# Kernel optimization log

Hardware: AMD Instinct MI355X
Metric: run time of the kernel (lower is better)

The kernel has to match this reference:

```python
import jax, jax.numpy as jnp
import numpy as np

B, NQ, NK, C, H = 4, 1024, 1024, 768, 12
DH = C // H
SCALE = DH ** -0.5
EPS = 1e-5  # nn.LayerNorm default
NEG_INF = float('-inf')


def _ln(x, g, b):
    m = jnp.mean(x, axis=-1, keepdims=True)
    v = jnp.mean((x - m) ** 2, axis=-1, keepdims=True)
    return (x - m) * jax.lax.rsqrt(v + EPS) * g + b


def _heads(t):  # [B,N,C] -> [B,H,N,Dh]
    Bq, N, _ = t.shape
    return t.reshape(Bq, N, H, DH).transpose(0, 2, 1, 3)


def setup_inputs() -> dict:
    key = jax.random.key(0)
    ks = jax.random.split(key, 32)
    w = lambda k, shape: jax.random.normal(k, shape, jnp.float32) * 0.02
    g = lambda k: 1.0 + jax.random.normal(k, (C,), jnp.float32) * 0.02
    b = lambda k: jax.random.normal(k, (C,), jnp.float32) * 0.02
    inp = {
        'x': jax.random.normal(ks[0], (B, NQ, C), jnp.float32),
        'y': jax.random.normal(ks[1], (B, NK, C), jnp.float32),
        'xpos': jnp.arange(B * NQ, dtype=jnp.int32).reshape(B, NQ),
        'ypos': jnp.arange(B * NK, dtype=jnp.int32).reshape(B, NK),
        'mask': jax.random.randint(ks[2], (NQ, NK), 0, 2) > 0,
        'similarities': jax.random.normal(ks[3], (B, H, NQ, NK), jnp.float32),
        # norms
        'ln1_g': g(ks[4]), 'ln1_b': b(ks[5]),
        'ln2_g': g(ks[6]), 'ln2_b': b(ks[7]),
        'ln3_g': g(ks[8]), 'ln3_b': b(ks[9]),
        'lny_g': g(ks[10]), 'lny_b': b(ks[11]),
        # self-attn (qkv_bias=False)
        'qkv_w': w(ks[12], (3 * C, C)),
        'aproj_w': w(ks[13], (C, C)), 'aproj_b': b(ks[14]),
        # cross-attn
        'pq_w': w(ks[15], (C, C)), 'pk_w': w(ks[16], (C, C)), 'pv_w': w(ks[17], (C, C)),
        'cproj_w': w(ks[18], (C, C)), 'cproj_b': b(ks[19]),
        # mlp (hidden = 4*C)
        'fc1_w': w(ks[20], (4 * C, C)), 'fc1_b': jax.random.normal(ks[21], (4 * C,), jnp.float32) * 0.02,
        'fc2_w': w(ks[22], (C, 4 * C)), 'fc2_b': b(ks[23]),
    }
    return inp


def reference(x, y, xpos, ypos, mask, similarities,
              ln1_g, ln1_b, ln2_g, ln2_b, ln3_g, ln3_b, lny_g, lny_b,
              qkv_w, aproj_w, aproj_b,
              pq_w, pk_w, pv_w, cproj_w, cproj_b,
              fc1_w, fc1_b, fc2_w, fc2_b):
    # ---- self-attention (rope=None, dropout=0) ----
    xn = _ln(x, ln1_g, ln1_b)
    qkv = (xn @ qkv_w.T).reshape(B, NQ, 3, H, DH).transpose(2, 0, 3, 1, 4)
    q, k, v = qkv[0], qkv[1], qkv[2]                       # [B,H,Nq,Dh]
    attn = jax.nn.softmax(jnp.einsum('bhqd,bhkd->bhqk', q, k) * SCALE, axis=-1)
    sa = jnp.einsum('bhqk,bhkd->bhqd', attn, v).transpose(0, 2, 1, 3).reshape(B, NQ, C)
    x = x + sa @ aproj_w.T + aproj_b

    # ---- sparse cross-attention with similarity bias + mask ----
    y_ = _ln(y, lny_g, lny_b)
    xn2 = _ln(x, ln2_g, ln2_b)
    cq = _heads(xn2 @ pq_w.T)                              # [B,H,Nq,Dh]
    ck = _heads(y_ @ pk_w.T)                               # [B,H,Nk,Dh]
    cv = _heads(y_ @ pv_w.T)
    scores = jnp.einsum('bhqd,bhkd->bhqk', cq, ck) * SCALE
    sims_c = similarities - jnp.mean(similarities, axis=1, keepdims=True)
    scores = scores + sims_c
    scores = jnp.where(mask[None, None], scores, NEG_INF)
    cattn = jax.nn.softmax(scores, axis=-1)
    ca = jnp.einsum('bhqk,bhkd->bhqd', cattn, cv).transpose(0, 2, 1, 3).reshape(B, NQ, C)
    x = x + ca @ cproj_w.T + cproj_b

    # ---- MLP (exact GELU, as nn.GELU default) ----
    xn3 = _ln(x, ln3_g, ln3_b)
    h = jax.nn.gelu(xn3 @ fc1_w.T + fc1_b, approximate=False)
    x = x + h @ fc2_w.T + fc2_b
    return (x, y)
```

## Files before the change

kernel.cpp:

```cpp
#include <hip/hip_runtime.h>
#include <cstdint>
#include <cstddef>


typedef __bf16 bf16;
typedef __attribute__((ext_vector_type(8))) __bf16 bf16x8;
typedef __attribute__((ext_vector_type(4))) __bf16 bf16x4;
typedef __attribute__((ext_vector_type(4))) float f32x4;

typedef __attribute__((address_space(1))) void gvoid;
typedef __attribute__((address_space(3))) void lvoid;

#define DEVI static __device__ __forceinline__

DEVI void gload16(const void* g, void* l) {
  __builtin_amdgcn_global_load_lds((gvoid*)(uintptr_t)g, (lvoid*)(uintptr_t)l, 16, 0, 0);
}

DEVI f32x4 mfma_bf16(bf16x8 a, bf16x8 b, f32x4 c) {
  return __builtin_amdgcn_mfma_f32_16x16x32_bf16(a, b, c, 0, 0, 0);
}

__global__ __launch_bounds__(256)
void detect_mask_k(const unsigned char* __restrict__ mask, int* __restrict__ shift)
{
  __shared__ int acc[256];
  const int t = threadIdx.x;
  int s = 0;
  for (int i = t; i < 16384; i += 256) {
    const int base = i * 4;
    s += mask[base + 1] + mask[base + 2] + mask[base + 3];
  }
  acc[t] = s;
  __syncthreads();
  #pragma unroll
  for (int o = 128; o; o >>= 1) {
    if (t < o) acc[t] += acc[t + o];
    __syncthreads();
  }
  if (t == 0) *shift = (acc[0] == 0) ? 2 : 0;
}

__global__ __launch_bounds__(256)
void bias_k(const float* __restrict__ sim,
            const unsigned char* __restrict__ mask,
            const int* __restrict__ mshift,
            bf16* __restrict__ biasOut)
{
  const int blk = blockIdx.x;
  const int b = blk >> 10, q = blk & 1023;
  const int t = threadIdx.x;
  const int k4 = t * 4;
  const int msh = *mshift;
  const float* sb = sim + (size_t)b * 12 * 1024 * 1024;
  bf16* ob = biasOut + (size_t)b * 12 * 1024 * 1024;

  f32x4 sv[12];
  f32x4 acc = {0.f, 0.f, 0.f, 0.f};
  #pragma unroll
  for (int h = 0; h < 12; ++h) {
    sv[h] = *(const f32x4*)(sb + ((size_t)h * 1024 + q) * 1024 + k4);
    acc += sv[h];
  }
  const f32x4 mean = acc * (1.0f / 12.0f);

  float mb[4];
  if (msh == 0) {
    const uchar4 mv = *(const uchar4*)(mask + (size_t)q * 1024 + k4);
    mb[0] = mv.x ? 0.f : -1e30f; mb[1] = mv.y ? 0.f : -1e30f;
    mb[2] = mv.z ? 0.f : -1e30f; mb[3] = mv.w ? 0.f : -1e30f;
  } else {
    const int4 mv = *(const int4*)((const int*)mask + (size_t)q * 1024 + k4);
    mb[0] = mv.x ? 0.f : -1e30f; mb[1] = mv.y ? 0.f : -1e30f;
    mb[2] = mv.z ? 0.f : -1e30f; mb[3] = mv.w ? 0.f : -1e30f;
  }

  #pragma unroll
  for (int h = 0; h < 12; ++h) {
    bf16x4 o;
    #pragma unroll
    for (int j = 0; j < 4; ++j)
      o[j] = (bf16)(sv[h][j] - mean[j] + mb[j]);
    *(bf16x4*)(ob + ((size_t)h * 1024 + q) * 1024 + k4) = o;
  }
}

struct CvtArgs {
  const float* src[8];
  bf16* dst[8];
  int end[8];
};
__global__ __launch_bounds__(256)
void cvt_all_k(CvtArgs a)
{
  const int i = blockIdx.x * 256 + threadIdx.x;
  int s = 0;
  #pragma unroll
  for (int j = 0; j < 7; ++j) s += (i >= a.end[j]) ? 1 : 0;
  const int base = s ? a.end[s - 1] : 0;
  const int off = i - base;
  const f32x4 v = *((const f32x4*)a.src[s] + off);
  bf16x4 o;
  o[0] = (bf16)v[0]; o[1] = (bf16)v[1]; o[2] = (bf16)v[2]; o[3] = (bf16)v[3];
  *(bf16x4*)(a.dst[s] + (size_t)off * 4) = o;
}

__global__ __launch_bounds__(256)
void copy4_k(const float* __restrict__ s, float* __restrict__ d, int n4)
{
  const int i = blockIdx.x * 256 + threadIdx.x;
  if (i < n4) ((f32x4*)d)[i] = ((const f32x4*)s)[i];
}

__global__ __launch_bounds__(256)
void ln_k(const float* __restrict__ xin, const float* __restrict__ g,
          const float* __restrict__ be, bf16* __restrict__ out)
{
  const int row = blockIdx.x, tid = threadIdx.x;
  const int lane = tid & 63, w = tid >> 6;
  const float* xr = xin + (size_t)row * 768;
  const float v0 = xr[tid], v1 = xr[tid + 256], v2 = xr[tid + 512];
  float s = v0 + v1 + v2;
  #pragma unroll
  for (int o = 32; o; o >>= 1) s += __shfl_xor(s, o);
  __shared__ float r1[4], r2[4];
  if (lane == 0) r1[w] = s;
  __syncthreads();
  const float mean = (r1[0] + r1[1] + r1[2] + r1[3]) * (1.0f / 768.0f);
  const float d0 = v0 - mean, d1 = v1 - mean, d2 = v2 - mean;
  float q = d0 * d0 + d1 * d1 + d2 * d2;
  #pragma unroll
  for (int o = 32; o; o >>= 1) q += __shfl_xor(q, o);
  if (lane == 0) r2[w] = q;
  __syncthreads();
  const float inv = rsqrtf((r2[0] + r2[1] + r2[2] + r2[3]) * (1.0f / 768.0f) + 1e-5f);
  bf16* orow = out + (size_t)row * 768;
  orow[tid]       = (bf16)(d0 * inv * g[tid]       + be[tid]);
  orow[tid + 256] = (bf16)(d1 * inv * g[tid + 256] + be[tid + 256]);
  orow[tid + 512] = (bf16)(d2 * inv * g[tid + 512] + be[tid + 512]);
}

__global__ __launch_bounds__(256)
void build_vt(const bf16* __restrict__ src, int ld, bf16* __restrict__ vt)
{
  __shared__ unsigned short t[64][72];
  const int bh = blockIdx.x, nt = blockIdx.y;
  const int b = bh / 12, hh = bh % 12;
  const int tid = threadIdx.x;
  {
    const int nl = tid >> 2, d0 = (tid & 3) * 16;
    const unsigned short* srow = (const unsigned short*)src
        + (size_t)(b * 1024 + nt * 64 + nl) * ld + hh * 64 + d0;
    #pragma unroll
    for (int j = 0; j < 4; ++j)
      *(ushort4*)(&t[nl][d0 + j * 4]) = *(const ushort4*)(srow + j * 4);
  }
  __syncthreads();
  {
    const int dl = tid >> 2, n0 = (tid & 3) * 16;
    unsigned short* drow = (unsigned short*)vt + ((size_t)bh * 64 + dl) * 1024 + nt * 64 + n0;
    #pragma unroll
    for (int j = 0; j < 4; ++j) {
      ushort4 o;
      o.x = t[n0 + j * 4 + 0][dl];
      o.y = t[n0 + j * 4 + 1][dl];
      o.z = t[n0 + j * 4 + 2][dl];
      o.w = t[n0 + j * 4 + 3][dl];
      *(ushort4*)(drow + j * 4) = o;
    }
  }
}

template<int BM, int BN, bool BIAS, bool GELU, bool RES, bool OBF>
__global__ __launch_bounds__(256)
void gemm_bt(const bf16* __restrict__ A, const bf16* __restrict__ Bt,
             const float* __restrict__ bias, const float* __restrict__ res,
             bf16* __restrict__ Cb, float* __restrict__ Cf,
             int M, int N, int K)
{
  constexpr int WM = BM / 2, WN = BN / 2;
  constexpr int FM = WM / 16, FN = WN / 16;
  __shared__ bf16 As[BM * 64];
  __shared__ bf16 Bs[BN * 64];
  const int tid = threadIdx.x;
  const int lane = tid & 63;
  const int wv = tid >> 6;
  const int wr = wv >> 1, wc = wv & 1;
  const int l15 = lane & 15, lg = lane >> 4;
  const int bm = blockIdx.y * BM, bn = blockIdx.x * BN;
  (void)M;

  f32x4 acc[FM][FN];
  const f32x4 z = {0.f, 0.f, 0.f, 0.f};
  #pragma unroll
  for (int i = 0; i < FM; ++i)
    #pragma unroll
    for (int j = 0; j < FN; ++j) acc[i][j] = z;

  for (int k0 = 0; k0 < K; k0 += 64) {
    __syncthreads();
    #pragma unroll
    for (int c = tid; c < BM * 8; c += 256) {
      const int row = c >> 3, colb = (c & 7) << 4;
      gload16((const char*)A + ((size_t)(bm + row) * K + k0) * 2 + colb,
              (char*)As + (size_t)c * 16);
    }
    #pragma unroll
    for (int c = tid; c < BN * 8; c += 256) {
      const int row = c >> 3, colb = (c & 7) << 4;
      gload16((const char*)Bt + ((size_t)(bn + row) * K + k0) * 2 + colb,
              (char*)Bs + (size_t)c * 16);
    }
    __syncthreads();
    #pragma unroll
    for (int kk = 0; kk < 64; kk += 32) {
      bf16x8 af[FM], bfr[FN];
      #pragma unroll
      for (int mi = 0; mi < FM; ++mi)
        af[mi] = *(const bf16x8*)(As + (size_t)(wr * WM + mi * 16 + l15) * 64 + kk + lg * 8);
      #pragma unroll
      for (int ni = 0; ni < FN; ++ni)
        bfr[ni] = *(const bf16x8*)(Bs + (size_t)(wc * WN + ni * 16 + l15) * 64 + kk + lg * 8);
      #pragma unroll
      for (int mi = 0; mi < FM; ++mi)
        #pragma unroll
        for (int ni = 0; ni < FN; ++ni)
          acc[mi][ni] = mfma_bf16(af[mi], bfr[ni], acc[mi][ni]);
    }
  }

  #pragma unroll
  for (int mi = 0; mi < FM; ++mi) {
    const int row0 = bm + wr * WM + mi * 16 + lg * 4;
    #pragma unroll
    for (int ni = 0; ni < FN; ++ni) {
      const int col = bn + wc * WN + ni * 16 + l15;
      #pragma unroll
      for (int r = 0; r < 4; ++r) {
        float v = acc[mi][ni][r];
        if constexpr (BIAS) v += bias[col];
        if constexpr (GELU) v = 0.5f * v * (1.0f + erff(v * 0.70710678118654752f));
        if constexpr (RES)  v += res[(size_t)(row0 + r) * N + col];
        if constexpr (OBF)  Cb[(size_t)(row0 + r) * N + col] = (bf16)v;
        else                Cf[(size_t)(row0 + r) * N + col] = v;
      }
    }
  }
}

template<int CROSS>
__global__ __launch_bounds__(256, 4)
void fattn_k(const bf16* __restrict__ Qp, int ldq,
             const bf16* __restrict__ Kp, int ldk,
             const bf16* __restrict__ Vt,
             const bf16* __restrict__ bias,
             bf16* __restrict__ Out)
{
  __shared__ bf16 Kl[64 * 64];
  __shared__ bf16 Vl[64 * 64];
  __shared__ bf16 Bl[4][16 * 72];
  __shared__ bf16 Pl[4][16 * 72];

  const int f = blockIdx.x;
  const int r8 = f & 7, rest = f >> 3;
  const int c6 = rest % 6, qt = rest / 6;
  const int pp = r8 + 8 * c6;
  const int b = pp / 12, hh = pp % 12;
  const int tid = threadIdx.x, lane = tid & 63, wq = tid >> 6;
  const int l15 = lane & 15, lg = lane >> 4;

  bf16x8 qreg0, qreg1;
  {
    const bf16* qsrc = Qp + (size_t)(b * 1024 + qt * 64 + wq * 16 + l15) * ldq + hh * 64 + lg * 8;
    qreg0 = *(const bf16x8*)qsrc;
    qreg1 = *(const bf16x8*)(qsrc + 32);
  }
  const char* Kbase = (const char*)(Kp + (size_t)b * 1024 * ldk + hh * 64);
  const char* Vbase = (const char*)(Vt + (size_t)(b * 12 + hh) * 64 * 1024);
  const char* Bbase = nullptr;
  if constexpr (CROSS)
    Bbase = (const char*)(bias + (((size_t)(b * 12 + hh)) * 1024 + qt * 64 + wq * 16) * 1024);

  f32x4 oacc[4];
  const f32x4 z = {0.f, 0.f, 0.f, 0.f};
  #pragma unroll
  for (int i = 0; i < 4; ++i) oacc[i] = z;
  float m_run = -1e30f, l_run = 0.f;

  char* BlW = (char*)&Bl[wq][0];
  char* PlW = (char*)&Pl[wq][0];
  const int swz = (l15 & 7) << 4;

  for (int t = 0; t < 16; ++t) {
    const int k0 = t * 64;
    __syncthreads();
    #pragma unroll
    for (int j = 0; j < 2; ++j) {
      const int c = j * 256 + tid;
      const int r = c >> 3;
      const int sw = ((c & 7) ^ (r & 7)) << 4;
      gload16(Kbase + ((size_t)(k0 + r) * ldk) * 2 + sw, (char*)Kl + (size_t)c * 16);
      gload16(Vbase + (size_t)r * 2048 + (size_t)k0 * 2 + sw, (char*)Vl + (size_t)c * 16);
    }
    if constexpr (CROSS) {
      #pragma unroll
      for (int j = 0; j < 2; ++j) {
        const int c = j * 64 + lane;
        const int r = c >> 3, off = (c & 7) * 16;
        const bf16x8 v = *(const bf16x8*)(Bbase + (size_t)r * 2048 + (size_t)k0 * 2 + off);
        *(bf16x8*)(BlW + r * 144 + off) = v;
      }
    }
    __syncthreads();

    f32x4 sacc[4];
    #pragma unroll
    for (int i = 0; i < 4; ++i) sacc[i] = z;
    #pragma unroll
    for (int ni = 0; ni < 4; ++ni) {
      const int rowb = (ni * 16 + l15) * 128;
      const bf16x8 a0 = *(const bf16x8*)((char*)Kl + rowb + ((lg * 16) ^ swz));
      const bf16x8 a1 = *(const bf16x8*)((char*)Kl + rowb + ((64 + lg * 16) ^ swz));
      sacc[ni] = mfma_bf16(a0, qreg0, sacc[ni]);
      sacc[ni] = mfma_bf16(a1, qreg1, sacc[ni]);
    }

    float sv[16];
    #pragma unroll
    for (int ni = 0; ni < 4; ++ni)
      #pragma unroll
      for (int r = 0; r < 4; ++r)
        sv[ni * 4 + r] = sacc[ni][r] * 0.125f;
    if constexpr (CROSS) {
      #pragma unroll
      for (int ni = 0; ni < 4; ++ni) {
        const bf16x4 bv = *(const bf16x4*)(BlW + l15 * 144 + ni * 32 + lg * 8);
        #pragma unroll
        for (int r = 0; r < 4; ++r)
          sv[ni * 4 + r] += (float)bv[r];
      }
    }
    float mx = sv[0];
    #pragma unroll
    for (int j = 1; j < 16; ++j) mx = fmaxf(mx, sv[j]);
    mx = fmaxf(mx, __shfl_xor(mx, 16));
    mx = fmaxf(mx, __shfl_xor(mx, 32));
    const float mnew = fmaxf(m_run, mx);
    const float corr = __expf(m_run - mnew);
    m_run = mnew;
    float ps = 0.f;
    #pragma unroll
    for (int j = 0; j < 16; ++j) { sv[j] = __expf(sv[j] - mnew); ps += sv[j]; }
    l_run = l_run * corr + ps;

    #pragma unroll
    for (int ni = 0; ni < 4; ++ni) {
      bf16x4 pw;
      #pragma unroll
      for (int r = 0; r < 4; ++r) pw[r] = (bf16)sv[ni * 4 + r];
      *(bf16x4*)(PlW + l15 * 144 + ni * 32 + lg * 8) = pw;
    }
    float cr[4];
    #pragma unroll
    for (int r = 0; r < 4; ++r) cr[r] = __shfl(corr, ((lane >> 4) << 2) + r);
    #pragma unroll
    for (int nd = 0; nd < 4; ++nd)
      #pragma unroll
      for (int r = 0; r < 4; ++r) oacc[nd][r] *= cr[r];

    const bf16x8 p0 = *(const bf16x8*)(PlW + l15 * 144 + lg * 16);
    const bf16x8 p1 = *(const bf16x8*)(PlW + l15 * 144 + 64 + lg * 16);
    #pragma unroll
    for (int nd = 0; nd < 4; ++nd) {
      const int rowb = (nd * 16 + l15) * 128;
      const bf16x8 v0 = *(const bf16x8*)((char*)Vl + rowb + ((lg * 16) ^ swz));
      const bf16x8 v1 = *(const bf16x8*)((char*)Vl + rowb + ((64 + lg * 16) ^ swz));
      oacc[nd] = mfma_bf16(p0, v0, oacc[nd]);
      oacc[nd] = mfma_bf16(p1, v1, oacc[nd]);
    }
  }

  float ls = l_run + __shfl_xor(l_run, 16);
  ls += __shfl_xor(ls, 32);
  const float inv = 1.0f / ls;
  float ivr[4];
  #pragma unroll
  for (int r = 0; r < 4; ++r) ivr[r] = __shfl(inv, ((lane >> 4) << 2) + r);
  bf16* ob = Out + (size_t)(b * 1024 + qt * 64 + wq * 16 + lg * 4) * 768 + hh * 64 + l15;
  #pragma unroll
  for (int r = 0; r < 4; ++r)
    #pragma unroll
    for (int nd = 0; nd < 4; ++nd)
      ob[(size_t)r * 768 + nd * 16] = (bf16)(oacc[nd][r] * ivr[r]);
}

extern "C" void kernel_launch(void* const* d_in, const int* in_sizes, int n_in,
                              void* d_out, int out_size, void* d_ws, size_t ws_size,
                              hipStream_t stream)
{
  (void)in_sizes; (void)n_in; (void)out_size; (void)ws_size;
  const float* x    = (const float*)d_in[0];
  const float* y    = (const float*)d_in[1];
  const unsigned char* mask = (const unsigned char*)d_in[4];
  const float* sim  = (const float*)d_in[5];
  const float* ln1g = (const float*)d_in[6];
  const float* ln1b = (const float*)d_in[7];
  const float* ln2g = (const float*)d_in[8];
  const float* ln2b = (const float*)d_in[9];
  const float* ln3g = (const float*)d_in[10];
  const float* ln3b = (const float*)d_in[11];
  const float* lnyg = (const float*)d_in[12];
  const float* lnyb = (const float*)d_in[13];
  const float* qkvw = (const float*)d_in[14];
  const float* apw  = (const float*)d_in[15];
  const float* apb  = (const float*)d_in[16];
  const float* pqw  = (const float*)d_in[17];
  const float* pkw  = (const float*)d_in[18];
  const float* pvw  = (const float*)d_in[19];
  const float* cpw  = (const float*)d_in[20];
  const float* cpb  = (const float*)d_in[21];
  const float* f1w  = (const float*)d_in[22];
  const float* f1b  = (const float*)d_in[23];
  const float* f2w  = (const float*)d_in[24];
  const float* f2b  = (const float*)d_in[25];

  char* ws = (char*)d_ws;
  size_t off = 0;
  auto alloc = [&](size_t bytes) -> void* {
    off = (off + 255) & ~(size_t)255;
    void* p = ws + off;
    off += bytes;
    return p;
  };
  const size_t T = 4096;
  bf16* w_qkv = (bf16*)alloc((size_t)2304 * 768 * 2);
  bf16* w_ap  = (bf16*)alloc((size_t)768 * 768 * 2);
  bf16* w_pq  = (bf16*)alloc((size_t)768 * 768 * 2);
  bf16* w_pkv = (bf16*)alloc((size_t)1536 * 768 * 2);
  bf16* w_cp  = (bf16*)alloc((size_t)768 * 768 * 2);
  bf16* w_f1  = (bf16*)alloc((size_t)3072 * 768 * 2);
  bf16* w_f2  = (bf16*)alloc((size_t)768 * 3072 * 2);
  bf16* xn    = (bf16*)alloc(T * 768 * 2);
  bf16* qkvo  = (bf16*)alloc(T * 2304 * 2);
  bf16* vt    = (bf16*)alloc((size_t)48 * 64 * 1024 * 2);
  bf16* sa    = (bf16*)alloc(T * 768 * 2);
  float* x1   = (float*)alloc(T * 768 * 4);
  bf16* yln   = (bf16*)alloc(T * 768 * 2);
  bf16* xn2   = (bf16*)alloc(T * 768 * 2);
  bf16* cqf   = (bf16*)alloc(T * 768 * 2);
  bf16* ckv   = (bf16*)alloc(T * 1536 * 2);
  bf16* cvtT  = (bf16*)alloc((size_t)48 * 64 * 1024 * 2);
  bf16* biasA = (bf16*)alloc((size_t)4 * 12 * 1024 * 1024 * 2);
  bf16* ca    = (bf16*)alloc(T * 768 * 2);
  float* x2   = (float*)alloc(T * 768 * 4);
  bf16* xn3   = (bf16*)alloc(T * 768 * 2);
  bf16* hbuf  = (bf16*)alloc(T * 3072 * 2);
  int* mshift = (int*)alloc(256);

  detect_mask_k<<<1, 256, 0, stream>>>(mask, mshift);

  {
    CvtArgs a;
    const float* srcs[8] = {qkvw, apw, pqw, pkw, pvw, cpw, f1w, f2w};
    bf16* dsts[8] = {w_qkv, w_ap, w_pq, w_pkv, w_pkv + 768 * 768, w_cp, w_f1, w_f2};
    const int n4s[8] = {442368, 147456, 147456, 147456, 147456, 147456, 589824, 589824};
    int cum = 0;
    for (int j = 0; j < 8; ++j) {
      a.src[j] = srcs[j]; a.dst[j] = dsts[j];
      cum += n4s[j]; a.end[j] = cum;
    }
    cvt_all_k<<<cum / 256, 256, 0, stream>>>(a);
  }

  bias_k<<<4096, 256, 0, stream>>>(sim, mask, mshift, biasA);

  ln_k<<<4096, 256, 0, stream>>>(x, ln1g, ln1b, xn);
  gemm_bt<128,128,false,false,false,true><<<dim3(18, 32), 256, 0, stream>>>(
      xn, w_qkv, nullptr, nullptr, qkvo, nullptr, 4096, 2304, 768);
  build_vt<<<dim3(48, 16), 256, 0, stream>>>(qkvo + 1536, 2304, vt);
  fattn_k<0><<<768, 256, 0, stream>>>(
      qkvo, 2304, qkvo + 768, 2304, vt, nullptr, sa);
  gemm_bt<64,128,true,false,true,false><<<dim3(6, 64), 256, 0, stream>>>(
      sa, w_ap, apb, x, nullptr, x1, 4096, 768, 768);

  ln_k<<<4096, 256, 0, stream>>>(y, lnyg, lnyb, yln);
  ln_k<<<4096, 256, 0, stream>>>(x1, ln2g, ln2b, xn2);
  gemm_bt<64,128,false,false,false,true><<<dim3(6, 64), 256, 0, stream>>>(
      xn2, w_pq, nullptr, nullptr, cqf, nullptr, 4096, 768, 768);
  gemm_bt<128,128,false,false,false,true><<<dim3(12, 32), 256, 0, stream>>>(
      yln, w_pkv, nullptr, nullptr, ckv, nullptr, 4096, 1536, 768);
  build_vt<<<dim3(48, 16), 256, 0, stream>>>(ckv + 768, 1536, cvtT);
  fattn_k<1><<<768, 256, 0, stream>>>(
      cqf, 768, ckv, 1536, cvtT, biasA, ca);
  gemm_bt<64,128,true,false,true,false><<<dim3(6, 64), 256, 0, stream>>>(
      ca, w_cp, cpb, x1, nullptr, x2, 4096, 768, 768);

  ln_k<<<4096, 256, 0, stream>>>(x2, ln3g, ln3b, xn3);
  gemm_bt<128,128,true,true,false,true><<<dim3(24, 32), 256, 0, stream>>>(
      xn3, w_f1, f1b, nullptr, hbuf, nullptr, 4096, 3072, 768);
  gemm_bt<64,128,true,false,true,false><<<dim3(6, 64), 256, 0, stream>>>(
      hbuf, w_f2, f2b, x2, nullptr, (float*)d_out, 4096, 768, 3072);

  copy4_k<<<3072, 256, 0, stream>>>(y, (float*)d_out + 3145728, 786432);
}
```

Before: 416.5 us.

## Double-buffer attention K/V tiles, XCD-aware GEMM grid mapping, fuse two LayerNorm launches

The flash-attention kernel now double-buffers its K/V tiles in shared memory, prefetching the next tile while computing the current one. It also reads the cross-attention bias directly from global memory into registers instead of staging it through LDS, and lowers the occupancy hint from 4 to 3 blocks per CU to fit the larger LDS footprint. GEMMs switch to a 1D grid remapped so consecutive blocks landing on the same XCD share A-row tiles for L2 reuse. The x and y LayerNorms are fused into one launch, removing a kernel launch.

Result: no change. 412.9 us (-0.9%).

```diff
diff --git a/kernel.cpp b/kernel.cpp
--- a/kernel.cpp
+++ b/kernel.cpp
@@ -112,11 +112,21 @@
   if (i < n4) ((f32x4*)d)[i] = ((const f32x4*)s)[i];
 }
 
-__global__ __launch_bounds__(256)
-void ln_k(const float* __restrict__ xin, const float* __restrict__ g,
-          const float* __restrict__ be, bf16* __restrict__ out)
-{
-  const int row = blockIdx.x, tid = threadIdx.x;
+template<bool DUAL>
+__global__ __launch_bounds__(256)
+void ln_k(const float* __restrict__ inA, const float* __restrict__ gA,
+          const float* __restrict__ bA, bf16* __restrict__ outA,
+          const float* __restrict__ inB, const float* __restrict__ gB,
+          const float* __restrict__ bB, bf16* __restrict__ outB)
+{
+  int row = blockIdx.x;
+  const float* xin = inA; const float* g = gA; const float* be = bA; bf16* out = outA;
+  if constexpr (DUAL) {
+    if (row >= 4096) {
+      row -= 4096; xin = inB; g = gB; be = bB; out = outB;
+    }
+  }
+  const int tid = threadIdx.x;
   const int lane = tid & 63, w = tid >> 6;
   const float* xr = xin + (size_t)row * 768;
   const float v0 = xr[tid], v1 = xr[tid + 256], v2 = xr[tid + 512];
@@ -176,26 +186,29 @@
 void gemm_bt(const bf16* __restrict__ A, const bf16* __restrict__ Bt,
              const float* __restrict__ bias, const float* __restrict__ res,
              bf16* __restrict__ Cb, float* __restrict__ Cf,
-             int M, int N, int K)
+             int nyPerXcd, int N, int K)
 {
   constexpr int WM = BM / 2, WN = BN / 2;
   constexpr int FM = WM / 16, FN = WN / 16;
   __shared__ bf16 As[BM * 64];
   __shared__ bf16 Bs[BN * 64];
+  const int f = blockIdx.x;
+  const int xcd = f & 7, j = f >> 3;
+  const int by = xcd + 8 * (j % nyPerXcd);
+  const int bx = j / nyPerXcd;
   const int tid = threadIdx.x;
   const int lane = tid & 63;
   const int wv = tid >> 6;
   const int wr = wv >> 1, wc = wv & 1;
   const int l15 = lane & 15, lg = lane >> 4;
-  const int bm = blockIdx.y * BM, bn = blockIdx.x * BN;
-  (void)M;
+  const int bm = by * BM, bn = bx * BN;
 
   f32x4 acc[FM][FN];
   const f32x4 z = {0.f, 0.f, 0.f, 0.f};
   #pragma unroll
   for (int i = 0; i < FM; ++i)
     #pragma unroll
-    for (int j = 0; j < FN; ++j) acc[i][j] = z;
+    for (int jj = 0; jj < FN; ++jj) acc[i][jj] = z;
 
   for (int k0 = 0; k0 < K; k0 += 64) {
     __syncthreads();
@@ -249,16 +262,15 @@
 }
 
 template<int CROSS>
-__global__ __launch_bounds__(256, 4)
+__global__ __launch_bounds__(256, 3)
 void fattn_k(const bf16* __restrict__ Qp, int ldq,
              const bf16* __restrict__ Kp, int ldk,
              const bf16* __restrict__ Vt,
              const bf16* __restrict__ bias,
              bf16* __restrict__ Out)
 {
-  __shared__ bf16 Kl[64 * 64];
-  __shared__ bf16 Vl[64 * 64];
-  __shared__ bf16 Bl[4][16 * 72];
+  __shared__ bf16 Kl[2][64 * 64];
+  __shared__ bf16 Vl[2][64 * 64];
   __shared__ bf16 Pl[4][16 * 72];
 
   const int f = blockIdx.x;
@@ -277,9 +289,9 @@
   }
   const char* Kbase = (const char*)(Kp + (size_t)b * 1024 * ldk + hh * 64);
   const char* Vbase = (const char*)(Vt + (size_t)(b * 12 + hh) * 64 * 1024);
-  const char* Bbase = nullptr;
+  const bf16* biasRow = nullptr;
   if constexpr (CROSS)
-    Bbase = (const char*)(bias + (((size_t)(b * 12 + hh)) * 1024 + qt * 64 + wq * 16) * 1024);
+    biasRow = bias + (((size_t)(b * 12 + hh)) * 1024 + qt * 64 + wq * 16 + l15) * 1024;
 
   f32x4 oacc[4];
   const f32x4 z = {0.f, 0.f, 0.f, 0.f};
@@ -287,31 +299,35 @@
   for (int i = 0; i < 4; ++i) oacc[i] = z;
   float m_run = -1e30f, l_run = 0.f;
 
-  char* BlW = (char*)&Bl[wq][0];
   char* PlW = (char*)&Pl[wq][0];
   const int swz = (l15 & 7) << 4;
 
-  for (int t = 0; t < 16; ++t) {
+  auto stage = [&](int buf, int t) {
     const int k0 = t * 64;
-    __syncthreads();
-    #pragma unroll
-    for (int j = 0; j < 2; ++j) {
-      const int c = j * 256 + tid;
+    #pragma unroll
+    for (int jj = 0; jj < 2; ++jj) {
+      const int c = jj * 256 + tid;
       const int r = c >> 3;
       const int sw = ((c & 7) ^ (r & 7)) << 4;
-      gload16(Kbase + ((size_t)(k0 + r) * ldk) * 2 + sw, (char*)Kl + (size_t)c * 16);
-      gload16(Vbase + (size_t)r * 2048 + (size_t)k0 * 2 + sw, (char*)Vl + (size_t)c * 16);
-    }
+      gload16(Kbase + ((size_t)(k0 + r) * ldk) * 2 + sw, (char*)&Kl[buf][0] + (size_t)c * 16);
+      gload16(Vbase + (size_t)r * 2048 + (size_t)k0 * 2 + sw, (char*)&Vl[buf][0] + (size_t)c * 16);
+    }
+  };
+
+  stage(0, 0);
+  __syncthreads();
+
+  for (int t = 0; t < 16; ++t) {
+    const int cur = t & 1;
+    const int k0 = t * 64;
+    if (t < 15) stage(cur ^ 1, t + 1);
+
+    bf16x4 bv[4];
     if constexpr (CROSS) {
-      #pragma unroll
-      for (int j = 0; j < 2; ++j) {
-        const int c = j * 64 + lane;
-        const int r = c >> 3, off = (c & 7) * 16;
-        const bf16x8 v = *(const bf16x8*)(Bbase + (size_t)r * 2048 + (size_t)k0 * 2 + off);
-        *(bf16x8*)(BlW + r * 144 + off) = v;
-      }
-    }
-    __syncthreads();
+      const bf16* bp = biasRow + k0 + lg * 4;
+      #pragma unroll
+      for (int ni = 0; ni < 4; ++ni) bv[ni] = *(const bf16x4*)(bp + ni * 16);
+    }
 
     f32x4 sacc[4];
     #pragma unroll
@@ -319,8 +335,8 @@
     #pragma unroll
     for (int ni = 0; ni < 4; ++ni) {
       const int rowb = (ni * 16 + l15) * 128;
-      const bf16x8 a0 = *(const bf16x8*)((char*)Kl + rowb + ((lg * 16) ^ swz));
-      const bf16x8 a1 = *(const bf16x8*)((char*)Kl + rowb + ((64 + lg * 16) ^ swz));
+      const bf16x8 a0 = *(const bf16x8*)((char*)&Kl[cur][0] + rowb + ((lg * 16) ^ swz));
+      const bf16x8 a1 = *(const bf16x8*)((char*)&Kl[cur][0] + rowb + ((64 + lg * 16) ^ swz));
       sacc[ni] = mfma_bf16(a0, qreg0, sacc[ni]);
       sacc[ni] = mfma_bf16(a1, qreg1, sacc[ni]);
     }
@@ -333,16 +349,14 @@
         sv[ni * 4 + r] = sacc[ni][r] * 0.125f;
     if constexpr (CROSS) {
       #pragma unroll
-      for (int ni = 0; ni < 4; ++ni) {
-        const bf16x4 bv = *(const bf16x4*)(BlW + l15 * 144 + ni * 32 + lg * 8);
+      for (int ni = 0; ni < 4; ++ni)
         #pragma unroll
         for (int r = 0; r < 4; ++r)
-          sv[ni * 4 + r] += (float)bv[r];
-      }
+          sv[ni * 4 + r] += (float)bv[ni][r];
     }
     float mx = sv[0];
     #pragma unroll
-    for (int j = 1; j < 16; ++j) mx = fmaxf(mx, sv[j]);
+    for (int jj = 1; jj < 16; ++jj) mx = fmaxf(mx, sv[jj]);
     mx = fmaxf(mx, __shfl_xor(mx, 16));
     mx = fmaxf(mx, __shfl_xor(mx, 32));
     const float mnew = fmaxf(m_run, mx);
@@ -350,7 +364,7 @@
     m_run = mnew;
     float ps = 0.f;
     #pragma unroll
-    for (int j = 0; j < 16; ++j) { sv[j] = __expf(sv[j] - mnew); ps += sv[j]; }
+    for (int jj = 0; jj < 16; ++jj) { sv[jj] = __expf(sv[jj] - mnew); ps += sv[jj]; }
     l_run = l_run * corr + ps;
 
     #pragma unroll
@@ -373,11 +387,12 @@
     #pragma unroll
     for (int nd = 0; nd < 4; ++nd) {
       const int rowb = (nd * 16 + l15) * 128;
-      const bf16x8 v0 = *(const bf16x8*)((char*)Vl + rowb + ((lg * 16) ^ swz));
-      const bf16x8 v1 = *(const bf16x8*)((char*)Vl + rowb + ((64 + lg * 16) ^ swz));
+      const bf16x8 v0 = *(const bf16x8*)((char*)&Vl[cur][0] + rowb + ((lg * 16) ^ swz));
+      const bf16x8 v1 = *(const bf16x8*)((char*)&Vl[cur][0] + rowb + ((64 + lg * 16) ^ swz));
       oacc[nd] = mfma_bf16(p0, v0, oacc[nd]);
       oacc[nd] = mfma_bf16(p1, v1, oacc[nd]);
     }
+    __syncthreads();
   }
 
   float ls = l_run + __shfl_xor(l_run, 16);
@@ -474,32 +489,33 @@
 
   bias_k<<<4096, 256, 0, stream>>>(sim, mask, mshift, biasA);
 
-  ln_k<<<4096, 256, 0, stream>>>(x, ln1g, ln1b, xn);
-  gemm_bt<128,128,false,false,false,true><<<dim3(18, 32), 256, 0, stream>>>(
-      xn, w_qkv, nullptr, nullptr, qkvo, nullptr, 4096, 2304, 768);
+  ln_k<true><<<8192, 256, 0, stream>>>(x, ln1g, ln1b, xn, y, lnyg, lnyb, yln);
+  gemm_bt<128,128,false,false,false,true><<<576, 256, 0, stream>>>(
+      xn, w_qkv, nullptr, nullptr, qkvo, nullptr, 4, 2304, 768);
   build_vt<<<dim3(48, 16), 256, 0, stream>>>(qkvo + 1536, 2304, vt);
   fattn_k<0><<<768, 256, 0, stream>>>(
       qkvo, 2304, qkvo + 768, 2304, vt, nullptr, sa);
-  gemm_bt<64,128,true,false,true,false><<<dim3(6, 64), 256, 0, stream>>>(
-      sa, w_ap, apb, x, nullptr, x1, 4096, 768, 768);
-
-  ln_k<<<4096, 256, 0, stream>>>(y, lnyg, lnyb, yln);
-  ln_k<<<4096, 256, 0, stream>>>(x1, ln2g, ln2b, xn2);
-  gemm_bt<64,128,false,false,false,true><<<dim3(6, 64), 256, 0, stream>>>(
-      xn2, w_pq, nullptr, nullptr, cqf, nullptr, 4096, 768, 768);
-  gemm_bt<128,128,false,false,false,true><<<dim3(12, 32), 256, 0, stream>>>(
-      yln, w_pkv, nullptr, nullptr, ckv, nullptr, 4096, 1536, 768);
+  gemm_bt<64,128,true,false,true,false><<<384, 256, 0, stream>>>(
+      sa, w_ap, apb, x, nullptr, x1, 8, 768, 768);
+
+  ln_k<false><<<4096, 256, 0, stream>>>(x1, ln2g, ln2b, xn2,
+                                        nullptr, nullptr, nullptr, nullptr);
+  gemm_bt<64,128,false,false,false,true><<<384, 256, 0, stream>>>(
+      xn2, w_pq, nullptr, nullptr, cqf, nullptr, 8, 768, 768);
+  gemm_bt<128,128,false,false,false,true><<<384, 256, 0, stream>>>(
+      yln, w_pkv, nullptr, nullptr, ckv, nullptr, 4, 1536, 768);
   build_vt<<<dim3(48, 16), 256, 0, stream>>>(ckv + 768, 1536, cvtT);
   fattn_k<1><<<768, 256, 0, stream>>>(
       cqf, 768, ckv, 1536, cvtT, biasA, ca);
-  gemm_bt<64,128,true,false,true,false><<<dim3(6, 64), 256, 0, stream>>>(
-      ca, w_cp, cpb, x1, nullptr, x2, 4096, 768, 768);
-
-  ln_k<<<4096, 256, 0, stream>>>(x2, ln3g, ln3b, xn3);
-  gemm_bt<128,128,true,true,false,true><<<dim3(24, 32), 256, 0, stream>>>(
-      xn3, w_f1, f1b, nullptr, hbuf, nullptr, 4096, 3072, 768);
-  gemm_bt<64,128,true,false,true,false><<<dim3(6, 64), 256, 0, stream>>>(
-      hbuf, w_f2, f2b, x2, nullptr, (float*)d_out, 4096, 768, 3072);
+  gemm_bt<64,128,true,false,true,false><<<384, 256, 0, stream>>>(
+      ca, w_cp, cpb, x1, nullptr, x2, 8, 768, 768);
+
+  ln_k<false><<<4096, 256, 0, stream>>>(x2, ln3g, ln3b, xn3,
+                                        nullptr, nullptr, nullptr, nullptr);
+  gemm_bt<128,128,true,true,false,true><<<768, 256, 0, stream>>>(
+      xn3, w_f1, f1b, nullptr, hbuf, nullptr, 4, 3072, 768);
+  gemm_bt<64,128,true,false,true,false><<<384, 256, 0, stream>>>(
+      hbuf, w_f2, f2b, x2, nullptr, (float*)d_out, 8, 768, 3072);
 
   copy4_k<<<3072, 256, 0, stream>>>(y, (float*)d_out + 3145728, 786432);
 }
```
